# Performance work log

Hardware: AMD Instinct MI355X
Metric: run time of the kernel (lower is better)

Reference implementation:

```python
import jax, jax.numpy as jnp
import numpy as np

N_HEAD = 16
ROPE_BASE = 10000.0


def rotate_half(x):
    d = x.shape[-1] // 2
    return jnp.concatenate((-x[..., d:], x[..., :d]), axis=-1)


def rope_cos_sin(T, head_dim, dtype):
    inv_freq = 1.0 / (ROPE_BASE ** (jnp.arange(0, head_dim, 2, dtype=jnp.float32) / head_dim))
    t = jnp.arange(T, dtype=jnp.float32)
    freqs = jnp.einsum('i,j->ij', t, inv_freq)  # [T, head_dim/2]
    emb = jnp.concatenate((freqs, freqs), axis=-1)  # [T, head_dim]
    return jnp.cos(emb).astype(dtype), jnp.sin(emb).astype(dtype)


def setup_inputs() -> dict:
    key = jax.random.key(0)
    k1, k2, k3 = jax.random.split(key, 3)
    B, T, C = 4, 2048, 2048
    x = jax.random.normal(k1, (B, T, C), dtype=jnp.float32)
    w_attn = jax.random.normal(k2, (3 * C, C), dtype=jnp.float32) * (1.0 / np.sqrt(C))
    w_proj = jax.random.normal(k3, (C, C), dtype=jnp.float32) * (1.0 / np.sqrt(C))
    return {"x": x, "w_attn": w_attn, "w_proj": w_proj}


def reference(x, w_attn, w_proj):
    B, T, C = x.shape
    H = N_HEAD
    D = C // H
    qkv = jnp.einsum('btc,fc->btf', x, w_attn)  # [B, T, 3C]
    q, k, v = jnp.split(qkv, 3, axis=-1)
    # [B, H, T, D]
    q = q.reshape(B, T, H, D).transpose(0, 2, 1, 3)
    k = k.reshape(B, T, H, D).transpose(0, 2, 1, 3)
    v = v.reshape(B, T, H, D).transpose(0, 2, 1, 3)
    cos, sin = rope_cos_sin(T, D, x.dtype)  # [T, D]
    cos = cos[None, None, :, :]
    sin = sin[None, None, :, :]
    q = q * cos + rotate_half(q) * sin
    k = k * cos + rotate_half(k) * sin
    # bidirectional SDPA
    scale = 1.0 / jnp.sqrt(jnp.asarray(D, dtype=x.dtype))
    att = jnp.einsum('bhtd,bhsd->bhts', q, k) * scale
    att = jax.nn.softmax(att, axis=-1)
    y = jnp.einsum('bhts,bhsd->bhtd', att, v)
    y = y.transpose(0, 2, 1, 3).reshape(B, T, C)
    return jnp.einsum('btc,oc->bto', y, w_proj)
```

## Files before the change

### kernel.cpp

```cpp
#include <hip/hip_runtime.h>

#define DEVINL __device__ __forceinline__

typedef unsigned short u16;
typedef __attribute__((ext_vector_type(8))) __bf16 bf16x8;
typedef __attribute__((ext_vector_type(4))) float f32x4;
typedef __attribute__((ext_vector_type(16))) float f32x16;

struct alignas(8) u16x4 { u16 x, y, z, w; };

#define MFMA16(a, b, c) __builtin_amdgcn_mfma_f32_16x16x32_bf16(a, b, c, 0, 0, 0)
#define MFMA32(a, b, c) __builtin_amdgcn_mfma_f32_32x32x16_bf16(a, b, c, 0, 0, 0)

DEVINL u16 f2bf(float f) {
  unsigned u = __builtin_bit_cast(unsigned, f);
  u += 0x7fffu + ((u >> 16) & 1u);
  return (u16)(u >> 16);
}

DEVINL unsigned cvtpk_bf16(float lo, float hi) {
  unsigned r;
  asm("v_cvt_pk_bf16_f32 %0, %1, %2" : "=v"(r) : "v"(lo), "v"(hi));
  return r;
}

DEVINL void plane_swap(unsigned& a, unsigned& b) {
  asm("v_permlane32_swap_b32 %0, %1" : "+v"(a), "+v"(b));
}

DEVINL void gload_lds16(const u16* g, u16* l) {
  __builtin_amdgcn_global_load_lds((const __attribute__((address_space(1))) void*)g,
                                   (__attribute__((address_space(3))) void*)l,
                                   16, 0, 0);
}

DEVINL bf16x8 frag64(const u16* lds, int row, int cg) {
  int c = cg ^ (row & 7);
  return *(const bf16x8*)(lds + row * 64 + c * 8);
}
DEVINL bf16x8 frag128(const u16* lds, int row, int cg) {
  int c = cg ^ (row & 7);
  return *(const bf16x8*)(lds + row * 128 + c * 8);
}

DEVINL void stage_k512(const u16* g, u16* lds, int wave, int lane) {
#pragma unroll
  for (int t = 0; t < 2; ++t) {
    int r = t * 32 + wave * 4 + (lane >> 4);
    int cg = (lane & 15) ^ (r & 7);
    gload_lds16(g + (size_t)r * 128 + cg * 8, lds + (t * 32 + wave * 4) * 128);
  }
}
DEVINL void stage_v512(const u16* g, int ldg, u16* lds, int wave, int lane) {
#pragma unroll
  for (int t = 0; t < 2; ++t) {
    int r = t * 64 + wave * 8 + (lane >> 3);
    int cg = (lane & 7) ^ (r & 7);
    gload_lds16(g + (size_t)r * ldg + cg * 8, lds + (t * 64 + wave * 8) * 64);
  }
}

DEVINL int perm32(int row) { return (row & 3) ^ ((row >> 2) & 3); }

DEVINL void stage32(const u16* g, int ldg, u16* lds, int q, int wave, int lane) {
  int row = q * 128 + wave * 16 + (lane >> 2);
  int cg = (lane & 3) ^ perm32(row);
  gload_lds16(g + (size_t)row * ldg + cg * 8, lds + (q * 128 + wave * 16) * 32);
}

DEVINL bf16x8 frag32(const u16* lds, int row, int lc) {
  int c = lc ^ perm32(row);
  return *(const bf16x8*)(lds + row * 32 + c * 8);
}

__global__ void __launch_bounds__(256) k_cast3(const float4* __restrict__ x,
                                               const float4* __restrict__ wa,
                                               const float4* __restrict__ wp,
                                               u16x4* __restrict__ xb,
                                               u16x4* __restrict__ wab,
                                               u16x4* __restrict__ wpb) {
  const int b = blockIdx.x;
  const float4* src;
  u16x4* dst;
  int n, i, stride;
  if (b < 1024) {
    src = x; dst = xb; n = 4194304;
    i = b * 256 + threadIdx.x; stride = 1024 * 256;
  } else if (b < 1792) {
    src = wa; dst = wab; n = 3145728;
    i = (b - 1024) * 256 + threadIdx.x; stride = 768 * 256;
  } else {
    src = wp; dst = wpb; n = 1048576;
    i = (b - 1792) * 256 + threadIdx.x; stride = 256 * 256;
  }
  for (; i < n; i += stride) {
    float4 f = src[i];
    u16x4 u;
    u.x = f2bf(f.x); u.y = f2bf(f.y); u.z = f2bf(f.z); u.w = f2bf(f.w);
    dst[i] = u;
  }
}

DEVINL void gemm_loop256(const u16* Ag, const u16* Bg, int K, u16* smem,
                         f32x4 acc[8][4], int wave, int lane) {
  const int wm = wave >> 2, wn = wave & 3;
  const int lr = lane & 15, lc = lane >> 4;

#pragma unroll
  for (int t = 0; t < 3; ++t) {
    u16* At = smem + t * 8192;
    u16* Bt = smem + 32768 + t * 8192;
    stage32(Ag + t * 32, K, At, 0, wave, lane);
    stage32(Ag + t * 32, K, At, 1, wave, lane);
    stage32(Bg + t * 32, K, Bt, 0, wave, lane);
    stage32(Bg + t * 32, K, Bt, 1, wave, lane);
  }
  asm volatile("s_waitcnt vmcnt(8)" ::: "memory");
  asm volatile("s_barrier" ::: "memory");

  bf16x8 bfr[4], aA[4], aB[4];
#pragma unroll
  for (int nf = 0; nf < 4; ++nf)
    bfr[nf] = frag32(smem + 32768, nf * 64 + wn * 16 + lr, lc);
#pragma unroll
  for (int mf = 0; mf < 4; ++mf)
    aA[mf] = frag32(smem, wm * 128 + mf * 16 + lr, lc);

  const int nsteps = K / 32;
  for (int s = 0; s < nsteps; ++s) {
    const int slot = s & 3;
    const u16* Ac = smem + slot * 8192;
    const bool do_stage = (s + 3 < nsteps);
    u16* An = smem + ((s + 3) & 3) * 8192;
    u16* Bn = smem + 32768 + ((s + 3) & 3) * 8192;
    const u16* Agn = Ag + (size_t)(s + 3) * 32;
    const u16* Bgn = Bg + (size_t)(s + 3) * 32;

    __builtin_amdgcn_s_setprio(1);
#pragma unroll
    for (int mf = 0; mf < 4; ++mf)
#pragma unroll
      for (int nf = 0; nf < 4; ++nf)
        acc[mf][nf] = MFMA16(aA[mf], bfr[nf], acc[mf][nf]);
    __builtin_amdgcn_s_setprio(0);
#pragma unroll
    for (int mf = 0; mf < 4; ++mf)
      aB[mf] = frag32(Ac, wm * 128 + (mf + 4) * 16 + lr, lc);
    if (do_stage) {
      stage32(Agn, K, An, 0, wave, lane);
      stage32(Agn, K, An, 1, wave, lane);
    }
    if (s + 3 < nsteps) {
      asm volatile("s_waitcnt vmcnt(6)" ::: "memory");
    } else if (s + 2 < nsteps) {
      asm volatile("s_waitcnt vmcnt(4)" ::: "memory");
    } else if (s + 1 < nsteps) {
      asm volatile("s_waitcnt vmcnt(0)" ::: "memory");
    }
    asm volatile("s_barrier" ::: "memory");

    __builtin_amdgcn_s_setprio(1);
#pragma unroll
    for (int mf = 0; mf < 4; ++mf)
#pragma unroll
      for (int nf = 0; nf < 4; ++nf)
        acc[mf + 4][nf] = MFMA16(aB[mf], bfr[nf], acc[mf + 4][nf]);
    __builtin_amdgcn_s_setprio(0);
    if (s + 1 < nsteps) {
      const int slot1 = (s + 1) & 3;
      const u16* An1 = smem + slot1 * 8192;
      const u16* Bn1 = smem + 32768 + slot1 * 8192;
#pragma unroll
      for (int nf = 0; nf < 4; ++nf)
        bfr[nf] = frag32(Bn1, nf * 64 + wn * 16 + lr, lc);
#pragma unroll
      for (int mf = 0; mf < 4; ++mf)
        aA[mf] = frag32(An1, wm * 128 + mf * 16 + lr, lc);
    }
    if (do_stage) {
      stage32(Bgn, K, Bn, 0, wave, lane);
      stage32(Bgn, K, Bn, 1, wave, lane);
    }
    asm volatile("s_barrier" ::: "memory");
  }
}

__global__ void __launch_bounds__(512, 2) k_gemm_qkv(const u16* __restrict__ xb,
                                                     const u16* __restrict__ wab,
                                                     u16* __restrict__ qb,
                                                     u16* __restrict__ kb,
                                                     u16* __restrict__ vtb) {
  extern __shared__ u16 smem[];
  int bid = blockIdx.x;
  const int xcd = bid & 7, local = bid >> 3;
  const int tm = (xcd & 3) * 8 + (local & 7);
  const int tn = (xcd >> 2) * 12 + (local >> 3);
  const int wave = threadIdx.x >> 6, lane = threadIdx.x & 63;
  const int wm = wave >> 2, wn = wave & 3;
  const int lr = lane & 15, lc = lane >> 4;

  f32x4 acc[8][4];
#pragma unroll
  for (int i = 0; i < 8; ++i)
#pragma unroll
    for (int n = 0; n < 4; ++n) acc[i][n] = f32x4{0.f, 0.f, 0.f, 0.f};

  gemm_loop256(xb + (size_t)tm * 256 * 2048, wab + (size_t)tn * 256 * 2048, 2048,
               smem, acc, wave, lane);

  const int sel = tn >> 3;
  const int hh = (tn & 7) * 2;
  const int m0 = tm * 256 + wm * 128;
  const int b = (tm * 256) >> 11;

  if (sel < 2) {
    u16* dst = sel ? kb : qb;
    const float qs = sel ? 1.0f : 0.12751745f;
    const int d = wn * 16 + lr;
    const float invf = __expf(-0.14391156631f * (float)d);
#pragma unroll
    for (int mf = 0; mf < 8; ++mf) {
#pragma unroll
      for (int j = 0; j < 4; ++j) {
        int t = (m0 + mf * 16 + lc * 4 + j) & 2047;
        float ang = (float)t * invf;
        float s, c;
        __sincosf(ang, &s, &c);
#pragma unroll
        for (int hp = 0; hp < 2; ++hp) {
          float lo = acc[mf][2 * hp][j];
          float hi = acc[mf][2 * hp + 1][j];
          size_t rowp = ((size_t)(b * 16 + hh + hp) * 2048 + t) * 128;
          dst[rowp + d] = f2bf((lo * c - hi * s) * qs);
          dst[rowp + d + 64] = f2bf((hi * c + lo * s) * qs);
        }
      }
    }
  } else {
#pragma unroll
    for (int mf = 0; mf < 8; ++mf) {
      int t0 = (m0 + mf * 16 + lc * 4) & 2047;
#pragma unroll
      for (int nf = 0; nf < 4; ++nf) {
        int d = wn * 16 + lr + (nf & 1) * 64;
        int h = hh + (nf >> 1);
        u16x4 pk;
        pk.x = f2bf(acc[mf][nf][0]);
        pk.y = f2bf(acc[mf][nf][1]);
        pk.z = f2bf(acc[mf][nf][2]);
        pk.w = f2bf(acc[mf][nf][3]);
        *(u16x4*)(vtb + ((size_t)(b * 16 + h) * 128 + d) * 2048 + t0) = pk;
      }
    }
  }
}

__global__ void __launch_bounds__(512, 2) k_gemm_proj(const u16* __restrict__ yb,
                                                      const u16* __restrict__ wpb,
                                                      float* __restrict__ out) {
  extern __shared__ u16 smem[];
  int bid = blockIdx.x;
  int sw = (bid & 7) * 32 + (bid >> 3);
  const int tm = sw >> 3, tn = sw & 7;
  const int wave = threadIdx.x >> 6, lane = threadIdx.x & 63;
  const int wm = wave >> 2, wn = wave & 3;
  const int lr = lane & 15, lc = lane >> 4;

  f32x4 acc[8][4];
#pragma unroll
  for (int i = 0; i < 8; ++i)
#pragma unroll
    for (int n = 0; n < 4; ++n) acc[i][n] = f32x4{0.f, 0.f, 0.f, 0.f};

  gemm_loop256(yb + (size_t)tm * 256 * 2048, wpb + (size_t)tn * 256 * 2048, 2048,
               smem, acc, wave, lane);

  const int m0 = tm * 256 + wm * 128;
#pragma unroll
  for (int mf = 0; mf < 8; ++mf) {
#pragma unroll
    for (int j = 0; j < 4; ++j) {
      int gr = m0 + mf * 16 + lc * 4 + j;
      float* op = out + (size_t)gr * 2048 + tn * 256 + wn * 16 + lr;
#pragma unroll
      for (int nf = 0; nf < 4; ++nf) op[nf * 64] = acc[mf][nf][j];
    }
  }
}

__global__ void __launch_bounds__(512, 4) k_attn(const u16* __restrict__ qg,
                                                 const u16* __restrict__ kg,
                                                 const u16* __restrict__ vtg,
                                                 u16* __restrict__ yg) {
  __shared__ u16 Ks[2][64 * 128];
  __shared__ u16 Vs[2][128 * 64];
  int bid = blockIdx.x;
  int sw = (bid & 7) * 64 + (bid >> 3);
  const int qt = sw & 7, bh = sw >> 3;
  const int wave = threadIdx.x >> 6, lane = threadIdx.x & 63;
  const int hi = lane >> 5, ln = lane & 31;

  const u16* qbh = qg + (size_t)bh * (2048 * 128);
  const u16* kbh = kg + (size_t)bh * (2048 * 128);
  const u16* vbh = vtg + (size_t)bh * (128 * 2048);
  const int qrow0 = qt * 256 + wave * 32;

  bf16x8 qf[8];
#pragma unroll
  for (int kc = 0; kc < 8; ++kc)
    qf[kc] = *(const bf16x8*)(qbh + (size_t)(qrow0 + ln) * 128 + kc * 16 + hi * 8);

  f32x16 yacc[4];
#pragma unroll
  for (int nd = 0; nd < 4; ++nd)
#pragma unroll
    for (int r = 0; r < 16; ++r) yacc[nd][r] = 0.f;
  float m = -1e30f, l = 0.f;

  stage_k512(kbh, Ks[0], wave, lane);
  stage_v512(vbh, 2048, Vs[0], wave, lane);
  __syncthreads();

  int buf = 0;
  for (int kv0 = 0; kv0 < 2048; kv0 += 64) {
    if (kv0 + 64 < 2048) {
      stage_k512(kbh + (size_t)(kv0 + 64) * 128, Ks[buf ^ 1], wave, lane);
      stage_v512(vbh + kv0 + 64, 2048, Vs[buf ^ 1], wave, lane);
    }
    const u16* Kb = Ks[buf];
    const u16* Vb = Vs[buf];

    f32x16 st[2];
#pragma unroll
    for (int h2 = 0; h2 < 2; ++h2)
#pragma unroll
      for (int r = 0; r < 16; ++r) st[h2][r] = 0.f;
    __builtin_amdgcn_s_setprio(1);
#pragma unroll
    for (int kc = 0; kc < 8; ++kc) {
      bf16x8 a0 = frag128(Kb, ln, kc * 2 + hi);
      bf16x8 a1 = frag128(Kb, 32 + ln, kc * 2 + hi);
      st[0] = MFMA32(a0, qf[kc], st[0]);
      st[1] = MFMA32(a1, qf[kc], st[1]);
    }
    __builtin_amdgcn_s_setprio(0);

    float t8[8];
#pragma unroll
    for (int i = 0; i < 8; ++i)
      t8[i] = fmaxf(fmaxf(st[0][i], st[0][i + 8]), fmaxf(st[1][i], st[1][i + 8]));
    float pmax = fmaxf(fmaxf(fmaxf(t8[0], t8[4]), fmaxf(t8[1], t8[5])),
                       fmaxf(fmaxf(t8[2], t8[6]), fmaxf(t8[3], t8[7])));
    pmax = fmaxf(pmax, __shfl_xor(pmax, 32));

    if (__any(pmax - m > 11.5415603f)) {
      float mn = fmaxf(m, pmax);
      float al = __builtin_amdgcn_exp2f(m - mn);
      m = mn;
      l *= al;
#pragma unroll
      for (int nd = 0; nd < 4; ++nd)
#pragma unroll
        for (int r = 0; r < 16; ++r) yacc[nd][r] *= al;
    }

    float sa0 = 0.f, sa1 = 0.f, sa2 = 0.f, sa3 = 0.f;
#pragma unroll
    for (int h2 = 0; h2 < 2; ++h2) {
#pragma unroll
      for (int r = 0; r < 16; ++r) {
        float e = __builtin_amdgcn_exp2f(st[h2][r] - m);
        st[h2][r] = e;
        if ((r & 3) == 0) sa0 += e;
        else if ((r & 3) == 1) sa1 += e;
        else if ((r & 3) == 2) sa2 += e;
        else sa3 += e;
      }
    }
    float ssum = (sa0 + sa1) + (sa2 + sa3);
    ssum += __shfl_xor(ssum, 32);
    l += ssum;

    unsigned wa[2][4], wb[2][4];
#pragma unroll
    for (int h2 = 0; h2 < 2; ++h2)
#pragma unroll
      for (int q8 = 0; q8 < 4; ++q8) {
        wa[h2][q8] = cvtpk_bf16(st[h2][q8 * 4 + 0], st[h2][q8 * 4 + 1]);
        wb[h2][q8] = cvtpk_bf16(st[h2][q8 * 4 + 2], st[h2][q8 * 4 + 3]);
      }

    __builtin_amdgcn_s_setprio(1);
#pragma unroll
    for (int ks = 0; ks < 4; ++ks) {
      const int h2 = ks >> 1, k1 = ks & 1;
      unsigned w0 = wa[h2][2 * k1], w2 = wa[h2][2 * k1 + 1];
      plane_swap(w0, w2);
      unsigned w1 = wb[h2][2 * k1], w3 = wb[h2][2 * k1 + 1];
      plane_swap(w1, w3);
      union { unsigned u[4]; bf16x8 v; } pa;
      pa.u[0] = w0; pa.u[1] = w1; pa.u[2] = w2; pa.u[3] = w3;
#pragma unroll
      for (int nd = 0; nd < 4; ++nd) {
        bf16x8 bv = frag64(Vb, nd * 32 + ln, 2 * ks + hi);
        yacc[nd] = MFMA32(pa.v, bv, yacc[nd]);
      }
    }
    __builtin_amdgcn_s_setprio(0);

    __syncthreads();
    buf ^= 1;
  }

  const int b = bh >> 4, h = bh & 15;
  float inv = 1.f / l;
#pragma unroll
  for (int r = 0; r < 16; ++r) {
    int crow = (r & 3) + 8 * (r >> 2) + 4 * hi;
    float li = __shfl(inv, crow);
    int t = qrow0 + crow;
    size_t rp = ((size_t)b * 2048 + t) * 2048 + h * 128;
#pragma unroll
    for (int nd = 0; nd < 4; ++nd)
      yg[rp + nd * 32 + ln] = f2bf(yacc[nd][r] * li);
  }
}

extern "C" void kernel_launch(void* const* d_in, const int* in_sizes, int n_in,
                              void* d_out, int out_size, void* d_ws, size_t ws_size,
                              hipStream_t stream) {
  const float* x = (const float*)d_in[0];
  const float* wa = (const float*)d_in[1];
  const float* wp = (const float*)d_in[2];
  float* out = (float*)d_out;

  u16* xb = (u16*)d_ws;
  u16* wab = xb + 16777216;
  u16* wpb = wab + 12582912;
  u16* qb = wpb + 4194304;
  u16* kb = qb + 16777216;
  u16* vtb = kb + 16777216;
  u16* yb = vtb + 16777216;

  hipFuncSetAttribute((const void*)k_gemm_qkv,
                      hipFuncAttributeMaxDynamicSharedMemorySize, 131072);
  hipFuncSetAttribute((const void*)k_gemm_proj,
                      hipFuncAttributeMaxDynamicSharedMemorySize, 131072);

  k_cast3<<<dim3(2048), dim3(256), 0, stream>>>(
      (const float4*)x, (const float4*)wa, (const float4*)wp,
      (u16x4*)xb, (u16x4*)wab, (u16x4*)wpb);
  k_gemm_qkv<<<dim3(768), dim3(512), 131072, stream>>>(xb, wab, qb, kb, vtb);
  k_attn<<<dim3(512), dim3(512), 0, stream>>>(qb, kb, vtb, yb);
  k_gemm_proj<<<dim3(256), dim3(512), 131072, stream>>>(yb, wpb, out);
}
```

Baseline: 527.2 us.

## Split 64-key attention step into two 32-key passes to cut register use

```diff
diff --git a/kernel.cpp b/kernel.cpp
--- a/kernel.cpp
+++ b/kernel.cpp
@@ -330,83 +330,76 @@
     const u16* Kb = Ks[buf];
     const u16* Vb = Vs[buf];
 
-    f32x16 st[2];
-#pragma unroll
-    for (int h2 = 0; h2 < 2; ++h2)
-#pragma unroll
-      for (int r = 0; r < 16; ++r) st[h2][r] = 0.f;
-    __builtin_amdgcn_s_setprio(1);
-#pragma unroll
-    for (int kc = 0; kc < 8; ++kc) {
-      bf16x8 a0 = frag128(Kb, ln, kc * 2 + hi);
-      bf16x8 a1 = frag128(Kb, 32 + ln, kc * 2 + hi);
-      st[0] = MFMA32(a0, qf[kc], st[0]);
-      st[1] = MFMA32(a1, qf[kc], st[1]);
-    }
-    __builtin_amdgcn_s_setprio(0);
-
-    float t8[8];
-#pragma unroll
-    for (int i = 0; i < 8; ++i)
-      t8[i] = fmaxf(fmaxf(st[0][i], st[0][i + 8]), fmaxf(st[1][i], st[1][i + 8]));
-    float pmax = fmaxf(fmaxf(fmaxf(t8[0], t8[4]), fmaxf(t8[1], t8[5])),
-                       fmaxf(fmaxf(t8[2], t8[6]), fmaxf(t8[3], t8[7])));
-    pmax = fmaxf(pmax, __shfl_xor(pmax, 32));
-
-    if (__any(pmax - m > 11.5415603f)) {
-      float mn = fmaxf(m, pmax);
-      float al = __builtin_amdgcn_exp2f(m - mn);
-      m = mn;
-      l *= al;
-#pragma unroll
-      for (int nd = 0; nd < 4; ++nd)
-#pragma unroll
-        for (int r = 0; r < 16; ++r) yacc[nd][r] *= al;
-    }
-
-    float sa0 = 0.f, sa1 = 0.f, sa2 = 0.f, sa3 = 0.f;
-#pragma unroll
+#pragma unroll 1
     for (int h2 = 0; h2 < 2; ++h2) {
+      f32x16 st;
+#pragma unroll
+      for (int r = 0; r < 16; ++r) st[r] = 0.f;
+      __builtin_amdgcn_s_setprio(1);
+#pragma unroll
+      for (int kc = 0; kc < 8; ++kc) {
+        bf16x8 a = frag128(Kb, h2 * 32 + ln, kc * 2 + hi);
+        st = MFMA32(a, qf[kc], st);
+      }
+      __builtin_amdgcn_s_setprio(0);
+
+      float t8[8];
+#pragma unroll
+      for (int i = 0; i < 8; ++i) t8[i] = fmaxf(st[i], st[i + 8]);
+      float pmax = fmaxf(fmaxf(fmaxf(t8[0], t8[4]), fmaxf(t8[1], t8[5])),
+                         fmaxf(fmaxf(t8[2], t8[6]), fmaxf(t8[3], t8[7])));
+      pmax = fmaxf(pmax, __shfl_xor(pmax, 32));
+
+      if (__any(pmax - m > 11.5415603f)) {
+        float mn = fmaxf(m, pmax);
+        float al = __builtin_amdgcn_exp2f(m - mn);
+        m = mn;
+        l *= al;
+#pragma unroll
+        for (int nd = 0; nd < 4; ++nd)
+#pragma unroll
+          for (int r = 0; r < 16; ++r) yacc[nd][r] *= al;
+      }
+
+      float sa0 = 0.f, sa1 = 0.f, sa2 = 0.f, sa3 = 0.f;
 #pragma unroll
       for (int r = 0; r < 16; ++r) {
-        float e = __builtin_amdgcn_exp2f(st[h2][r] - m);
-        st[h2][r] = e;
+        float e = __builtin_amdgcn_exp2f(st[r] - m);
+        st[r] = e;
         if ((r & 3) == 0) sa0 += e;
         else if ((r & 3) == 1) sa1 += e;
         else if ((r & 3) == 2) sa2 += e;
         else sa3 += e;
       }
-    }
-    float ssum = (sa0 + sa1) + (sa2 + sa3);
-    ssum += __shfl_xor(ssum, 32);
-    l += ssum;
-
-    unsigned wa[2][4], wb[2][4];
-#pragma unroll
-    for (int h2 = 0; h2 < 2; ++h2)
+      float ssum = (sa0 + sa1) + (sa2 + sa3);
+      ssum += __shfl_xor(ssum, 32);
+      l += ssum;
+
+      unsigned wa[4], wb[4];
 #pragma unroll
       for (int q8 = 0; q8 < 4; ++q8) {
-        wa[h2][q8] = cvtpk_bf16(st[h2][q8 * 4 + 0], st[h2][q8 * 4 + 1]);
-        wb[h2][q8] = cvtpk_bf16(st[h2][q8 * 4 + 2], st[h2][q8 * 4 + 3]);
-      }
-
-    __builtin_amdgcn_s_setprio(1);
-#pragma unroll
-    for (int ks = 0; ks < 4; ++ks) {
-      const int h2 = ks >> 1, k1 = ks & 1;
-      unsigned w0 = wa[h2][2 * k1], w2 = wa[h2][2 * k1 + 1];
-      plane_swap(w0, w2);
-      unsigned w1 = wb[h2][2 * k1], w3 = wb[h2][2 * k1 + 1];
-      plane_swap(w1, w3);
-      union { unsigned u[4]; bf16x8 v; } pa;
-      pa.u[0] = w0; pa.u[1] = w1; pa.u[2] = w2; pa.u[3] = w3;
-#pragma unroll
-      for (int nd = 0; nd < 4; ++nd) {
-        bf16x8 bv = frag64(Vb, nd * 32 + ln, 2 * ks + hi);
-        yacc[nd] = MFMA32(pa.v, bv, yacc[nd]);
-      }
-    }
-    __builtin_amdgcn_s_setprio(0);
+        wa[q8] = cvtpk_bf16(st[q8 * 4 + 0], st[q8 * 4 + 1]);
+        wb[q8] = cvtpk_bf16(st[q8 * 4 + 2], st[q8 * 4 + 3]);
+      }
+
+      __builtin_amdgcn_s_setprio(1);
+#pragma unroll
+      for (int k1 = 0; k1 < 2; ++k1) {
+        unsigned w0 = wa[2 * k1], w2 = wa[2 * k1 + 1];
+        plane_swap(w0, w2);
+        unsigned w1 = wb[2 * k1], w3 = wb[2 * k1 + 1];
+        plane_swap(w1, w3);
+        union { unsigned u[4]; bf16x8 v; } pa;
+        pa.u[0] = w0; pa.u[1] = w1; pa.u[2] = w2; pa.u[3] = w3;
+        const int cgv = 2 * (2 * h2 + k1) + hi;
+#pragma unroll
+        for (int nd = 0; nd < 4; ++nd) {
+          bf16x8 bv = frag64(Vb, nd * 32 + ln, cgv);
+          yacc[nd] = MFMA32(pa.v, bv, yacc[nd]);
+        }
+      }
+      __builtin_amdgcn_s_setprio(0);
+    }
 
     __syncthreads();
     buf ^= 1;
```

Measured after the change: 533.8 us. About the same (+1.2%).
